# Kernel tuning notes

Hardware: AMD Instinct MI355X
Metric: run time of the kernel (lower is better)

Reference implementation:

```python
import jax, jax.numpy as jnp
import numpy as np

B, N, U = 4, 4096, 512


def setup_inputs() -> dict:
    key = jax.random.key(0)
    ks = jax.random.split(key, 5)
    s = 1.0 / np.sqrt(U)
    return {
        "x": jax.random.normal(ks[0], (B, N, U), dtype=jnp.float32),
        "Wq": jax.random.normal(ks[1], (U, U), dtype=jnp.float32) * s,
        "bq": jnp.zeros((U,), dtype=jnp.float32),
        "Wk": jax.random.normal(ks[2], (U, U), dtype=jnp.float32) * s,
        "bk": jnp.zeros((U,), dtype=jnp.float32),
        "Wv": jax.random.normal(ks[3], (U, U), dtype=jnp.float32) * s,
        "bv": jnp.zeros((U,), dtype=jnp.float32),
        "Wp": jax.random.normal(ks[4], (U, U), dtype=jnp.float32) * s,
        "bp": jnp.zeros((U,), dtype=jnp.float32),
    }


def reference(x, Wq, bq, Wk, bk, Wv, bv, Wp, bp):
    # x: [B, N, U] single-head self-attention with residual
    scale = jnp.asarray(x.shape[-1], jnp.float32) ** -0.5
    q = x @ Wq + bq
    k = x @ Wk + bk
    v = x @ Wv + bv
    scores = jnp.einsum("bnd,bmd->bnm", q, k) * scale  # [B, N, N]
    attn = jax.nn.softmax(scores, axis=-1)
    ctx = jnp.einsum("bnm,bmd->bnd", attn, v)
    return x + (ctx @ Wp + bp)
```

## Files before the change

### kernel.cpp

```cpp
#include <hip/hip_runtime.h>
#include <hip/hip_bf16.h>
#include <math.h>

#define NB 4
#define NN 4096
#define UU 512

using short8   = __attribute__((ext_vector_type(8))) short;
using bf16x8   = __attribute__((ext_vector_type(8))) __bf16;
using floatx4  = __attribute__((ext_vector_type(4))) float;
using floatx16 = __attribute__((ext_vector_type(16))) float;

__device__ __forceinline__ floatx4 mfma16(short8 a, short8 b, floatx4 c) {
    return __builtin_amdgcn_mfma_f32_16x16x32_bf16(
        __builtin_bit_cast(bf16x8, a), __builtin_bit_cast(bf16x8, b), c, 0, 0, 0);
}
__device__ __forceinline__ floatx4 mfma16f8(long a, long b, floatx4 c) {
    return __builtin_amdgcn_mfma_f32_16x16x32_fp8_fp8(a, b, c, 0, 0, 0);
}
__device__ __forceinline__ floatx16 mfma32f8(long a, long b, floatx16 c) {
    return __builtin_amdgcn_mfma_f32_32x32x16_fp8_fp8(a, b, c, 0, 0, 0);
}

__device__ __forceinline__ unsigned short f2bf(float f) {
    union { float f; unsigned u; } v; v.f = f;
    return (unsigned short)((v.u + 0x7fffu + ((v.u >> 16) & 1u)) >> 16);
}
__device__ __forceinline__ float bf2f(unsigned short s) {
    union { unsigned u; float f; } v; v.u = ((unsigned)s) << 16; return v.f;
}
template <bool HI>
__device__ __forceinline__ int cvtpk8(float a, float b, int old) {
    return __builtin_amdgcn_cvt_pk_fp8_f32(a, b, old, HI);
}

#define GLL16(gp, lp) __builtin_amdgcn_global_load_lds( \
    (const __attribute__((address_space(1))) void*)(gp), \
    (__attribute__((address_space(3))) void*)(lp), 16, 0, 0)

__global__ void __launch_bounds__(256) k_cvt_x(const float* __restrict__ x,
                                               unsigned short* __restrict__ xb) {
    int i = (blockIdx.x * 256 + threadIdx.x) * 4;
    float4 v = *(const float4*)(x + i);
    ushort4 o;
    o.x = f2bf(v.x); o.y = f2bf(v.y); o.z = f2bf(v.z); o.w = f2bf(v.w);
    *(ushort4*)(xb + i) = o;
}

__global__ void __launch_bounds__(256) k_cvt_w4(
    const float* __restrict__ W0, const float* __restrict__ W1,
    const float* __restrict__ W2, const float* __restrict__ W3,
    unsigned short* __restrict__ T0, unsigned short* __restrict__ T1,
    unsigned short* __restrict__ T2, unsigned short* __restrict__ T3) {
    const int z = blockIdx.z;
    const float* W = (z == 0) ? W0 : (z == 1) ? W1 : (z == 2) ? W2 : W3;
    unsigned short* T = (z == 0) ? T0 : (z == 1) ? T1 : (z == 2) ? T2 : T3;
    int idx = blockIdx.x * 256 + threadIdx.x;
    int n = idx >> 9, k = idx & 511;
    T[idx] = f2bf(W[k * 512 + n]);
}

__global__ void __launch_bounds__(256, 2) k_proj(
    const unsigned short* __restrict__ Xb,
    const unsigned short* __restrict__ WqT, const unsigned short* __restrict__ WkT,
    const unsigned short* __restrict__ WvT,
    const float* __restrict__ bq, const float* __restrict__ bk, const float* __restrict__ bv,
    unsigned char* __restrict__ Q, unsigned char* __restrict__ K8,
    unsigned char* __restrict__ V8)
{
    __shared__ __align__(16) unsigned short As[128 * 32];
    __shared__ __align__(16) unsigned short Bs[128 * 32];
    const int z = blockIdx.z;
    const unsigned short* WT = (z == 0) ? WqT : (z == 1) ? WkT : WvT;
    const float* bias = (z == 0) ? bq : (z == 1) ? bk : bv;
    const int t = threadIdx.x, wave = t >> 6, lane = t & 63;
    const int quad = lane >> 4, l16 = lane & 15;
    const int m0 = blockIdx.x * 128, n0 = blockIdx.y * 128;
    const int wm = wave >> 1, wn = wave & 1;

    const int srow = wave * 32 + (lane >> 2);
    const int scol = (lane & 3) * 8;
    const unsigned short* gA = Xb + (size_t)(m0 + srow) * UU + scol;
    const unsigned short* gB = WT + (size_t)(n0 + srow) * UU + scol;
    unsigned short* lA = As + wave * 1024;
    unsigned short* lB = Bs + wave * 1024;

    floatx4 acc[4][4] = {};

    for (int k0 = 0; k0 < UU; k0 += 32) {
        GLL16(gA + k0, lA);
        GLL16(gA + k0 + 16 * UU, lA + 512);
        GLL16(gB + k0, lB);
        GLL16(gB + k0 + 16 * UU, lB + 512);
        __syncthreads();
        short8 a[4], b[4];
        #pragma unroll
        for (int i = 0; i < 4; i++)
            a[i] = *(const short8*)(As + (wm * 64 + i * 16 + l16) * 32 + quad * 8);
        #pragma unroll
        for (int j = 0; j < 4; j++)
            b[j] = *(const short8*)(Bs + (wn * 64 + j * 16 + l16) * 32 + quad * 8);
        #pragma unroll
        for (int i = 0; i < 4; i++)
            #pragma unroll
            for (int j = 0; j < 4; j++)
                acc[i][j] = mfma16(a[i], b[j], acc[i][j]);
        __syncthreads();
    }

    #pragma unroll
    for (int j = 0; j < 4; j++) {
        const int n = n0 + wn * 64 + j * 16 + l16;
        const float bv_ = bias[n];
        #pragma unroll
        for (int i = 0; i < 4; i++) {
            const int mb = m0 + wm * 64 + i * 16 + quad * 4;
            const int bb = mb >> 12, tok = mb & (NN - 1);
            int d = cvtpk8<false>(acc[i][j][0] + bv_, acc[i][j][1] + bv_, 0);
            d     = cvtpk8<true>(acc[i][j][2] + bv_, acc[i][j][3] + bv_, d);
            if (z == 0) {
                #pragma unroll
                for (int r = 0; r < 4; r++)
                    Q[(size_t)(mb + r) * UU + n]
                        = (unsigned char)(((unsigned)d >> (8 * r)) & 0xffu);
            } else if (z == 1) {
                const size_t base = (size_t)bb * NN * UU + (size_t)(n >> 3) * (NN * 8)
                                  + (size_t)tok * 8 + (n & 7);
                #pragma unroll
                for (int r = 0; r < 4; r++)
                    K8[base + (size_t)r * 8]
                        = (unsigned char)(((unsigned)d >> (8 * r)) & 0xffu);
            } else {
                *(unsigned int*)(V8 + (size_t)bb * NN * UU + (size_t)(tok >> 3) * (UU * 8)
                                 + (size_t)n * 8 + (tok & 7)) = (unsigned)d;
            }
        }
    }
}

__global__ void __launch_bounds__(512, 1) k_flash(
    const unsigned char* __restrict__ Q,
    const unsigned char* __restrict__ K8,
    const unsigned char* __restrict__ V8,
    unsigned short* __restrict__ ctx)
{
    __shared__ __align__(16) unsigned char Ks[64 * 64 * 8];
    __shared__ __align__(16) unsigned char Vs[8 * 512 * 8];
    __shared__ __align__(16) float S_lds[64 * 68];
    __shared__ __align__(16) unsigned char P_lds8[64 * 72];
    __shared__ float m_lds[64], l_lds[64], a_lds[64];

    const int b = blockIdx.y;
    const int q0 = blockIdx.x * 64;
    const int t = threadIdx.x;
    const int wave = t >> 6, lane = t & 63, quad = lane >> 4, l16 = lane & 15;
    const int qt = wave >> 1;
    const int kh = wave & 1;
    const int qh = wave >> 2;
    const int dg = wave & 3;
    const int l31 = lane & 31, hi = lane >> 5;

    if (t < 64) { m_lds[t] = -INFINITY; l_lds[t] = 0.f; }

    const unsigned char* qp = Q + (size_t)(b * NN + q0 + qt * 16 + l16) * UU + quad * 8;
    long qf[16];
    #pragma unroll
    for (int kk = 0; kk < 16; kk++) qf[kk] = *(const long*)(qp + kk * 32);

    const unsigned char* K8b = K8 + (size_t)b * NN * UU;
    const unsigned char* V8b = V8 + (size_t)b * NN * UU;

    #pragma unroll
    for (int j = 0; j < 4; j++) {
        const int dc = wave * 8 + j * 2;
        GLL16(K8b + (size_t)(dc + (lane >> 5)) * (NN * 8) + (size_t)((lane & 31) * 2) * 8,
              Ks + dc * 512 + lane * 16);
    }

    floatx16 o[4] = {};
    const float sscale = 0.04419417382415922f * 1.4426950408889634f;

    __syncthreads();

    for (int kt = 0; kt < NN; kt += 64) {
        #pragma unroll
        for (int j = 0; j < 4; j++) {
            const int c = wave * 4 + j;
            GLL16(V8b + (size_t)kt * 512 + (size_t)c * 1024 + lane * 16,
                  Vs + c * 1024 + lane * 16);
        }

        floatx4 s0 = {}, s1 = {};
        #pragma unroll
        for (int kk = 0; kk < 16; kk++) {
            const unsigned char* kb = Ks + ((kk * 4 + quad) * 64 + kh * 32 + l16) * 8;
            long b0 = *(const long*)(kb);
            long b1 = *(const long*)(kb + 128);
            s0 = mfma16f8(qf[kk], b0, s0);
            s1 = mfma16f8(qf[kk], b1, s1);
        }
        #pragma unroll
        for (int i = 0; i < 4; i++) {
            S_lds[(qt * 16 + quad * 4 + i) * 68 + kh * 32 + l16]      = s0[i] * sscale;
            S_lds[(qt * 16 + quad * 4 + i) * 68 + kh * 32 + 16 + l16] = s1[i] * sscale;
        }
        __syncthreads();

        if (kt + 64 < NN) {
            #pragma unroll
            for (int j = 0; j < 4; j++) {
                const int dc = wave * 8 + j * 2;
                GLL16(K8b + (size_t)(dc + (lane >> 5)) * (NN * 8)
                          + (size_t)(kt + 64 + (lane & 31) * 2) * 8,
                      Ks + dc * 512 + lane * 16);
            }
        }

        {
            const int row = t >> 3, c8 = (t & 7) * 8;
            const float4* sp = (const float4*)(S_lds + row * 68 + c8);
            float4 va = sp[0], vb = sp[1];
            float mx = fmaxf(fmaxf(fmaxf(va.x, va.y), fmaxf(va.z, va.w)),
                             fmaxf(fmaxf(vb.x, vb.y), fmaxf(vb.z, vb.w)));
            mx = fmaxf(mx, __shfl_xor(mx, 1, 8));
            mx = fmaxf(mx, __shfl_xor(mx, 2, 8));
            mx = fmaxf(mx, __shfl_xor(mx, 4, 8));
            const float m_old = m_lds[row];
            const float m_new = fmaxf(m_old, mx);
            int d0 = cvtpk8<false>(exp2f(va.x - m_new), exp2f(va.y - m_new), 0);
            d0     = cvtpk8<true>(exp2f(va.z - m_new), exp2f(va.w - m_new), d0);
            int d1 = cvtpk8<false>(exp2f(vb.x - m_new), exp2f(vb.y - m_new), 0);
            d1     = cvtpk8<true>(exp2f(vb.z - m_new), exp2f(vb.w - m_new), d1);
            *(uint2*)(P_lds8 + row * 72 + c8) = make_uint2((unsigned)d0, (unsigned)d1);
            float sum = __builtin_amdgcn_cvt_f32_fp8(d0, 0)
                      + __builtin_amdgcn_cvt_f32_fp8(d0, 1)
                      + __builtin_amdgcn_cvt_f32_fp8(d0, 2)
                      + __builtin_amdgcn_cvt_f32_fp8(d0, 3)
                      + __builtin_amdgcn_cvt_f32_fp8(d1, 0)
                      + __builtin_amdgcn_cvt_f32_fp8(d1, 1)
                      + __builtin_amdgcn_cvt_f32_fp8(d1, 2)
                      + __builtin_amdgcn_cvt_f32_fp8(d1, 3);
            sum += __shfl_xor(sum, 1, 8);
            sum += __shfl_xor(sum, 2, 8);
            sum += __shfl_xor(sum, 4, 8);
            if ((t & 7) == 0) {
                const float alpha = exp2f(m_old - m_new);
                a_lds[row] = alpha;
                m_lds[row] = m_new;
                l_lds[row] = l_lds[row] * alpha + sum;
            }
        }
        __syncthreads();

        {
            float4 al4[4];
            #pragma unroll
            for (int r1 = 0; r1 < 4; r1++)
                al4[r1] = *(const float4*)(a_lds + qh * 32 + hi * 4 + r1 * 8);
            bool nr = false;
            #pragma unroll
            for (int r1 = 0; r1 < 4; r1++)
                nr = nr | (al4[r1].x != 1.f) | (al4[r1].y != 1.f)
                        | (al4[r1].z != 1.f) | (al4[r1].w != 1.f);
            if (__any(nr)) {
                #pragma unroll
                for (int tt = 0; tt < 4; tt++)
                    #pragma unroll
                    for (int r = 0; r < 16; r++)
                        o[tt][r] *= al4[r >> 2][r & 3];
            }

            long aP[4];
            #pragma unroll
            for (int ks = 0; ks < 4; ks++)
                aP[ks] = *(const long*)(P_lds8 + (qh * 32 + l31) * 72 + ks * 16 + hi * 8);
            #pragma unroll
            for (int ks = 0; ks < 4; ks++) {
                #pragma unroll
                for (int tt = 0; tt < 4; tt++) {
                    const int d0 = dg * 128 + tt * 32;
                    long bV = *(const long*)(Vs + (ks * 2 + hi) * 4096
                                             + (size_t)(d0 + l31) * 8);
                    o[tt] = mfma32f8(aP[ks], bV, o[tt]);
                }
            }
        }
        __syncthreads();
    }

    float4 li4[4];
    #pragma unroll
    for (int r1 = 0; r1 < 4; r1++) {
        float4 lv = *(const float4*)(l_lds + qh * 32 + hi * 4 + r1 * 8);
        li4[r1] = make_float4(1.f / lv.x, 1.f / lv.y, 1.f / lv.z, 1.f / lv.w);
    }
    #pragma unroll
    for (int tt = 0; tt < 4; tt++) {
        const int d0 = dg * 128 + tt * 32;
        #pragma unroll
        for (int r = 0; r < 16; r++) {
            const int row = q0 + qh * 32 + (r & 3) + 8 * (r >> 2) + 4 * hi;
            ctx[(size_t)(b * NN + row) * UU + d0 + l31]
                = f2bf(o[tt][r] * ((const float*)&li4[r >> 2])[r & 3]);
        }
    }
}

__global__ void __launch_bounds__(256, 2) k_out(
    const unsigned short* __restrict__ Cx,
    const unsigned short* __restrict__ WpT,
    const float* __restrict__ bp,
    const float* __restrict__ x,
    float* __restrict__ out)
{
    __shared__ __align__(16) unsigned short As[128 * 32];
    __shared__ __align__(16) unsigned short Bs[128 * 32];
    const int t = threadIdx.x, wave = t >> 6, lane = t & 63;
    const int quad = lane >> 4, l16 = lane & 15;
    const int m0 = blockIdx.x * 128, n0 = blockIdx.y * 128;
    const int wm = wave >> 1, wn = wave & 1;
    const int srow = wave * 32 + (lane >> 2);
    const int scol = (lane & 3) * 8;
    const unsigned short* gA = Cx + (size_t)(m0 + srow) * UU + scol;
    const unsigned short* gB = WpT + (size_t)(n0 + srow) * UU + scol;
    unsigned short* lA = As + wave * 1024;
    unsigned short* lB = Bs + wave * 1024;

    floatx4 acc[4][4] = {};

    for (int k0 = 0; k0 < UU; k0 += 32) {
        GLL16(gA + k0, lA);
        GLL16(gA + k0 + 16 * UU, lA + 512);
        GLL16(gB + k0, lB);
        GLL16(gB + k0 + 16 * UU, lB + 512);
        __syncthreads();
        short8 a[4], b[4];
        #pragma unroll
        for (int i = 0; i < 4; i++)
            a[i] = *(const short8*)(As + (wm * 64 + i * 16 + l16) * 32 + quad * 8);
        #pragma unroll
        for (int j = 0; j < 4; j++)
            b[j] = *(const short8*)(Bs + (wn * 64 + j * 16 + l16) * 32 + quad * 8);
        #pragma unroll
        for (int i = 0; i < 4; i++)
            #pragma unroll
            for (int j = 0; j < 4; j++)
                acc[i][j] = mfma16(a[i], b[j], acc[i][j]);
        __syncthreads();
    }

    #pragma unroll
    for (int j = 0; j < 4; j++) {
        const int n = n0 + wn * 64 + j * 16 + l16;
        const float bv_ = bp[n];
        #pragma unroll
        for (int i = 0; i < 4; i++) {
            const int mb = m0 + wm * 64 + i * 16 + quad * 4;
            #pragma unroll
            for (int r = 0; r < 4; r++) {
                const size_t idx = (size_t)(mb + r) * UU + n;
                out[idx] = acc[i][j][r] + bv_ + x[idx];
            }
        }
    }
}

extern "C" void kernel_launch(void* const* d_in, const int* in_sizes, int n_in,
                              void* d_out, int out_size, void* d_ws, size_t ws_size,
                              hipStream_t stream)
{
    const float* x  = (const float*)d_in[0];
    const float* Wq = (const float*)d_in[1];
    const float* bq = (const float*)d_in[2];
    const float* Wk = (const float*)d_in[3];
    const float* bk = (const float*)d_in[4];
    const float* Wv = (const float*)d_in[5];
    const float* bv = (const float*)d_in[6];
    const float* Wp = (const float*)d_in[7];
    const float* bp = (const float*)d_in[8];
    float* out = (float*)d_out;

    char* ws = (char*)d_ws;
    unsigned short* Xb  = (unsigned short*)(ws);
    unsigned short* WqT = (unsigned short*)(ws + 16777216);
    unsigned short* WkT = (unsigned short*)(ws + 17301504);
    unsigned short* WvT = (unsigned short*)(ws + 17825792);
    unsigned short* WpT = (unsigned short*)(ws + 18350080);
    unsigned char*  Qm  = (unsigned char*)(ws + 18874368);
    unsigned char*  K8m = (unsigned char*)(ws + 35651584);
    unsigned char*  V8m = (unsigned char*)(ws + 52428800);
    unsigned short* Cx  = (unsigned short*)(ws + 69206016);

    hipLaunchKernelGGL(k_cvt_x, dim3(8192), dim3(256), 0, stream, x, Xb);
    hipLaunchKernelGGL(k_cvt_w4, dim3(1024, 1, 4), dim3(256), 0, stream,
                       Wq, Wk, Wv, Wp, WqT, WkT, WvT, WpT);
    hipLaunchKernelGGL(k_proj, dim3(128, 4, 3), dim3(256), 0, stream,
                       Xb, WqT, WkT, WvT, bq, bk, bv, Qm, K8m, V8m);
    hipLaunchKernelGGL(k_flash, dim3(64, 4), dim3(512), 0, stream, Qm, K8m, V8m, Cx);
    hipLaunchKernelGGL(k_out, dim3(128, 4), dim3(256), 0, stream, Cx, WpT, bp, x, out);
}
```

Baseline: 336.1 us.

## Stage projection epilogue in LDS for coalesced stores and merge convert kernels

The projection kernel now writes its fp8 results into a 16KB shared tile laid out in the Q/K/V target format, then copies it to global memory with 16-byte vector stores. This replaces scattered byte-wide global stores. The x and weight conversion kernels are also merged into one launch, saving a kernel launch. In exchange, the extra shared memory may lower occupancy of the projection kernel, and the epilogue gains an extra barrier.

```diff
diff --git a/kernel.cpp b/kernel.cpp
--- a/kernel.cpp
+++ b/kernel.cpp
@@ -38,26 +38,29 @@
     (const __attribute__((address_space(1))) void*)(gp), \
     (__attribute__((address_space(3))) void*)(lp), 16, 0, 0)
 
-__global__ void __launch_bounds__(256) k_cvt_x(const float* __restrict__ x,
-                                               unsigned short* __restrict__ xb) {
-    int i = (blockIdx.x * 256 + threadIdx.x) * 4;
-    float4 v = *(const float4*)(x + i);
-    ushort4 o;
-    o.x = f2bf(v.x); o.y = f2bf(v.y); o.z = f2bf(v.z); o.w = f2bf(v.w);
-    *(ushort4*)(xb + i) = o;
-}
-
-__global__ void __launch_bounds__(256) k_cvt_w4(
+__global__ void __launch_bounds__(256) k_cvt(
+    const float* __restrict__ x, unsigned short* __restrict__ xb,
     const float* __restrict__ W0, const float* __restrict__ W1,
     const float* __restrict__ W2, const float* __restrict__ W3,
     unsigned short* __restrict__ T0, unsigned short* __restrict__ T1,
-    unsigned short* __restrict__ T2, unsigned short* __restrict__ T3) {
-    const int z = blockIdx.z;
-    const float* W = (z == 0) ? W0 : (z == 1) ? W1 : (z == 2) ? W2 : W3;
-    unsigned short* T = (z == 0) ? T0 : (z == 1) ? T1 : (z == 2) ? T2 : T3;
-    int idx = blockIdx.x * 256 + threadIdx.x;
-    int n = idx >> 9, k = idx & 511;
-    T[idx] = f2bf(W[k * 512 + n]);
+    unsigned short* __restrict__ T2, unsigned short* __restrict__ T3)
+{
+    const int bid = blockIdx.x;
+    if (bid < 8192) {
+        int i = (bid * 256 + threadIdx.x) * 4;
+        float4 v = *(const float4*)(x + i);
+        ushort4 o;
+        o.x = f2bf(v.x); o.y = f2bf(v.y); o.z = f2bf(v.z); o.w = f2bf(v.w);
+        *(ushort4*)(xb + i) = o;
+    } else {
+        int idx = (bid - 8192) * 256 + threadIdx.x;
+        int n = idx >> 9, k = idx & 511;
+        const int src = k * 512 + n;
+        T0[idx] = f2bf(W0[src]);
+        T1[idx] = f2bf(W1[src]);
+        T2[idx] = f2bf(W2[src]);
+        T3[idx] = f2bf(W3[src]);
+    }
 }
 
 __global__ void __launch_bounds__(256, 2) k_proj(
@@ -70,6 +73,7 @@
 {
     __shared__ __align__(16) unsigned short As[128 * 32];
     __shared__ __align__(16) unsigned short Bs[128 * 32];
+    __shared__ __align__(16) unsigned char Rs[128 * 128];
     const int z = blockIdx.z;
     const unsigned short* WT = (z == 0) ? WqT : (z == 1) ? WkT : WvT;
     const float* bias = (z == 0) ? bq : (z == 1) ? bk : bv;
@@ -110,31 +114,53 @@
 
     #pragma unroll
     for (int j = 0; j < 4; j++) {
-        const int n = n0 + wn * 64 + j * 16 + l16;
-        const float bv_ = bias[n];
+        const int nl = wn * 64 + j * 16 + l16;
+        const float bv_ = bias[n0 + nl];
         #pragma unroll
         for (int i = 0; i < 4; i++) {
-            const int mb = m0 + wm * 64 + i * 16 + quad * 4;
-            const int bb = mb >> 12, tok = mb & (NN - 1);
+            const int ml = wm * 64 + i * 16 + quad * 4;
             int d = cvtpk8<false>(acc[i][j][0] + bv_, acc[i][j][1] + bv_, 0);
             d     = cvtpk8<true>(acc[i][j][2] + bv_, acc[i][j][3] + bv_, d);
             if (z == 0) {
                 #pragma unroll
                 for (int r = 0; r < 4; r++)
-                    Q[(size_t)(mb + r) * UU + n]
-                        = (unsigned char)(((unsigned)d >> (8 * r)) & 0xffu);
+                    Rs[(ml + r) * 128 + nl] = (unsigned char)(((unsigned)d >> (8 * r)) & 0xffu);
             } else if (z == 1) {
-                const size_t base = (size_t)bb * NN * UU + (size_t)(n >> 3) * (NN * 8)
-                                  + (size_t)tok * 8 + (n & 7);
                 #pragma unroll
                 for (int r = 0; r < 4; r++)
-                    K8[base + (size_t)r * 8]
+                    Rs[(nl >> 3) * 1024 + (ml + r) * 8 + (nl & 7)]
                         = (unsigned char)(((unsigned)d >> (8 * r)) & 0xffu);
             } else {
-                *(unsigned int*)(V8 + (size_t)bb * NN * UU + (size_t)(tok >> 3) * (UU * 8)
-                                 + (size_t)n * 8 + (tok & 7)) = (unsigned)d;
-            }
-        }
+                *(unsigned int*)(Rs + (ml >> 3) * 1024 + nl * 8 + (ml & 7)) = (unsigned)d;
+            }
+        }
+    }
+    __syncthreads();
+
+    const int bb = m0 >> 12, tok0 = m0 & (NN - 1);
+    if (z == 0) {
+        const int row = t >> 1, off = (t & 1) * 64;
+        const unsigned char* src = Rs + row * 128 + off;
+        unsigned char* dst = Q + (size_t)(m0 + row) * UU + n0 + off;
+        #pragma unroll
+        for (int u = 0; u < 4; u++)
+            *(uint4*)(dst + u * 16) = *(const uint4*)(src + u * 16);
+    } else if (z == 1) {
+        const int c = t >> 4, seg = (t & 15) * 64;
+        const unsigned char* src = Rs + c * 1024 + seg;
+        unsigned char* dst = K8 + (size_t)bb * NN * UU
+                           + (size_t)((n0 >> 3) + c) * (NN * 8) + (size_t)tok0 * 8 + seg;
+        #pragma unroll
+        for (int u = 0; u < 4; u++)
+            *(uint4*)(dst + u * 16) = *(const uint4*)(src + u * 16);
+    } else {
+        const int c = t >> 4, seg = (t & 15) * 64;
+        const unsigned char* src = Rs + c * 1024 + seg;
+        unsigned char* dst = V8 + (size_t)bb * NN * UU
+                           + (size_t)((tok0 >> 3) + c) * (UU * 8) + (size_t)n0 * 8 + seg;
+        #pragma unroll
+        for (int u = 0; u < 4; u++)
+            *(uint4*)(dst + u * 16) = *(const uint4*)(src + u * 16);
     }
 }
 
@@ -391,9 +417,8 @@
     unsigned char*  V8m = (unsigned char*)(ws + 52428800);
     unsigned short* Cx  = (unsigned short*)(ws + 69206016);
 
-    hipLaunchKernelGGL(k_cvt_x, dim3(8192), dim3(256), 0, stream, x, Xb);
-    hipLaunchKernelGGL(k_cvt_w4, dim3(1024, 1, 4), dim3(256), 0, stream,
-                       Wq, Wk, Wv, Wp, WqT, WkT, WvT, WpT);
+    hipLaunchKernelGGL(k_cvt, dim3(9216), dim3(256), 0, stream,
+                       x, Xb, Wq, Wk, Wv, Wp, WqT, WkT, WvT, WpT);
     hipLaunchKernelGGL(k_proj, dim3(128, 4, 3), dim3(256), 0, stream,
                        Xb, WqT, WkT, WvT, bq, bk, bv, Qm, K8m, V8m);
     hipLaunchKernelGGL(k_flash, dim3(64, 4), dim3(512), 0, stream, Qm, K8m, V8m, Cx);
```

New measurement: 339.7 us. Within noise of the previous version (+1.1%).
